# Kernel optimization log

Hardware: AMD Instinct MI355X
Metric: run time of the kernel (lower is better)

## Reference

```python
import jax, jax.numpy as jnp
import numpy as np

ENC_DIM = 512
QUERY_DIM = 1024
ATTN_DIM = 128
CONV_CH = 32
KERNEL = 31
B, T = 64, 2048


def setup_inputs() -> dict:
    key = jax.random.key(0)
    ks = jax.random.split(key, 9)
    s = 0.02
    encoder_outputs = jax.random.normal(ks[0], (B, T, ENC_DIM), dtype=jnp.float32)
    decoder_hidden = jax.random.normal(ks[1], (B, QUERY_DIM), dtype=jnp.float32)
    prev_attention = jax.random.uniform(ks[2], (B, T), dtype=jnp.float32)
    prev_attention = prev_attention / jnp.sum(prev_attention, axis=1, keepdims=True)
    Wq = jax.random.normal(ks[3], (QUERY_DIM, ATTN_DIM), dtype=jnp.float32) * s
    Wk = jax.random.normal(ks[4], (ENC_DIM, ATTN_DIM), dtype=jnp.float32) * s
    conv_w = jax.random.normal(ks[5], (CONV_CH, 1, KERNEL), dtype=jnp.float32) * s  # OIH
    conv_b = jax.random.normal(ks[6], (CONV_CH,), dtype=jnp.float32) * s
    Wloc = jax.random.normal(ks[7], (CONV_CH, ATTN_DIM), dtype=jnp.float32) * s
    v = jax.random.normal(ks[8], (ATTN_DIM,), dtype=jnp.float32) * s
    return {"encoder_outputs": encoder_outputs, "decoder_hidden": decoder_hidden,
            "prev_attention": prev_attention, "Wq": Wq, "Wk": Wk,
            "conv_w": conv_w, "conv_b": conv_b, "Wloc": Wloc, "v": v}


def reference(encoder_outputs, decoder_hidden, prev_attention, Wq, Wk, conv_w, conv_b, Wloc, v):
    # query: [B, 1, A]
    query = (decoder_hidden @ Wq)[:, None, :]
    # keys: [B, T, A]
    keys = jnp.einsum('bte,ea->bta', encoder_outputs, Wk)
    # location conv: prev_attention [B, T] -> [B, 1, T] -> [B, C, T], SAME padding
    pad = (KERNEL - 1) // 2
    loc = jax.lax.conv_general_dilated(
        prev_attention[:, None, :], conv_w,
        window_strides=(1,), padding=[(pad, pad)],
        dimension_numbers=('NCH', 'OIH', 'NCH'))
    loc = loc + conv_b[None, :, None]
    # [B, T, C] -> [B, T, A]
    location_term = jnp.einsum('bct,ca->bta', loc, Wloc)
    energy = jnp.einsum('bta,a->bt', jnp.tanh(keys + query + location_term), v)
    return jax.nn.softmax(energy, axis=1)
```

## Files before the change

### kernel.cpp

```cpp
#include <hip/hip_runtime.h>
#include <hip/hip_bf16.h>

#define B_  64
#define T_  2048
#define E_  512
#define Q_  1024
#define A_  128
#define C_  32
#define KW_ 31

using bf16x8 = __attribute__((ext_vector_type(8))) short;
using f32x4  = __attribute__((ext_vector_type(4))) float;

__device__ __forceinline__ short f2bf(float f) {
  union { float f; unsigned u; } x; x.f = f;
  unsigned r = x.u + 0x7fffu + ((x.u >> 16) & 1u);
  return (short)(r >> 16);
}

__device__ __forceinline__ bf16x8 pack8(float4 a, float4 b) {
  union { bf16x8 v; __hip_bfloat162 h[4]; } u;
  u.h[0] = __float22bfloat162_rn(make_float2(a.x, a.y));
  u.h[1] = __float22bfloat162_rn(make_float2(a.z, a.w));
  u.h[2] = __float22bfloat162_rn(make_float2(b.x, b.y));
  u.h[3] = __float22bfloat162_rn(make_float2(b.z, b.w));
  return u.v;
}

__device__ __forceinline__ float fast_tanh(float x) {
  float e2 = __expf(2.f * x);
  return 1.f - 2.f * __builtin_amdgcn_rcpf(e2 + 1.f);
}

__device__ __forceinline__ void gload16(const void* g, void* l) {
  __builtin_amdgcn_global_load_lds(
      (const __attribute__((address_space(1))) unsigned int*)g,
      (__attribute__((address_space(3))) unsigned int*)l, 16, 0, 0);
}

__global__ __launch_bounds__(256) void prep_kernel(
    const float* __restrict__ dh, const float* __restrict__ Wq,
    const float* __restrict__ conv_b, const float* __restrict__ Wloc,
    const float* __restrict__ Wk,
    unsigned short* __restrict__ wkf, unsigned short* __restrict__ wlocf,
    float* __restrict__ q2p)
{
  int blk = blockIdx.x;
  int tid = threadIdx.x;
  if (blk < 512) {
    __shared__ float part[128];
    int b = blk >> 3, kq = blk & 7;
    int a = tid & 127, kh = tid >> 7;
    const float* dhr = dh + b * Q_ + kq * 128 + kh * 64;
    const float* wq  = Wq + (size_t)(kq * 128 + kh * 64) * A_ + a;
    float s = 0.f;
    #pragma unroll 8
    for (int k = 0; k < 64; ++k) s += dhr[k] * wq[(size_t)k * A_];
    if (kh) part[a] = s;
    __syncthreads();
    if (!kh) {
      s += part[a];
      if (kq == 0) {
        float t = 0.f;
        #pragma unroll 8
        for (int c = 0; c < C_; ++c) t += conv_b[c] * Wloc[c * A_ + a];
        s += t;
      }
      q2p[(kq * B_ + b) * A_ + a] = s;
    }
  } else if (blk < 544) {
    int wave = tid >> 6, lane = tid & 63;
    int g = (blk - 512) * 4 + wave;
    int ks = g >> 3, nt = g & 7;
    int lg = lane >> 4, lr = lane & 15;
    bf16x8 o;
    #pragma unroll
    for (int j = 0; j < 8; ++j)
      o[j] = f2bf(Wk[(ks * 32 + lg * 8 + j) * A_ + nt * 16 + lr]);
    *(bf16x8*)(wkf + ((size_t)g * 64 + lane) * 8) = o;
  } else {
    int wave = tid >> 6, lane = tid & 63;
    int g = (blk - 544) * 4 + wave;
    int lg = lane >> 4, lr = lane & 15;
    bf16x8 o;
    #pragma unroll
    for (int j = 0; j < 8; ++j)
      o[j] = f2bf(Wloc[(lg * 8 + j) * A_ + g * 16 + lr]);
    *(bf16x8*)(wlocf + ((size_t)g * 64 + lane) * 8) = o;
  }
}

__global__ __launch_bounds__(256, 4) void energy_kernel(
    const float* __restrict__ enc, const float* __restrict__ prev,
    const float* __restrict__ conv_w,
    const unsigned short* __restrict__ wkfall,
    const float* __restrict__ q2p, const float* __restrict__ vvec,
    float* __restrict__ outexp, float* __restrict__ psum)
{
  __shared__ unsigned short sB0[4096];
  __shared__ unsigned short sB1[4096];
  __shared__ float sprev[160];
  __shared__ float scw[KW_][C_];
  __shared__ unsigned short slocb[128][C_];
  __shared__ float swsum[4];

  int tid = threadIdx.x;
  int m0 = blockIdx.x * 128;
  int b  = m0 >> 11, t0 = m0 & (T_ - 1);

  for (int i = tid; i < 158; i += 256) {
    int t = t0 - 15 + i;
    sprev[i] = (t >= 0 && t < T_) ? prev[b * T_ + t] : 0.f;
  }
  for (int i = tid; i < KW_ * C_; i += 256) {
    int j = i >> 5, c = i & 31;
    scw[j][c] = conv_w[c * KW_ + j];
  }
  __syncthreads();
  {
    int tl = tid >> 1, ch0 = (tid & 1) * 16;
    float acc[16];
    #pragma unroll
    for (int c = 0; c < 16; ++c) acc[c] = 0.f;
    for (int j = 0; j < KW_; ++j) {
      float p = sprev[tl + j];
      #pragma unroll
      for (int c = 0; c < 16; ++c) acc[c] += p * scw[j][ch0 + c];
    }
    unsigned int* dstp = (unsigned int*)&slocb[tl][ch0];
    #pragma unroll
    for (int c = 0; c < 16; c += 2)
      dstp[c >> 1] = ((unsigned int)(unsigned short)f2bf(acc[c + 1]) << 16)
                   | (unsigned short)f2bf(acc[c]);
  }
  __syncthreads();

  int wave = tid >> 6, lane = tid & 63;
  int lg = lane >> 4, lr = lane & 15;
  int wm = m0 + wave * 32;

  const float* encRow0 = enc + (size_t)(wm + lr) * E_ + lg * 8;
  const float* encRow1 = encRow0 + 16 * E_;

  #define STAGE(slice, buf) do {                                              \
    const unsigned short* s_ = wkfall + (size_t)(slice) * 4096 + wave * 512 + lane * 8; \
    gload16(s_,        &buf[wave * 512]);                                     \
    gload16(s_ + 2048, &buf[(4 + wave) * 512]);                               \
  } while (0)

  f32x4 acc0[8], acc1[8];
  #pragma unroll
  for (int i = 0; i < 8; ++i) { acc0[i] = (f32x4){0,0,0,0}; acc1[i] = (f32x4){0,0,0,0}; }

  float4 aA0, aA1, aA2, aA3, aB0, aB1, aB2, aB3;

  STAGE(0, sB0);
  __builtin_amdgcn_sched_barrier(0);
  aA0 = *(const float4*)(encRow0);     aA1 = *(const float4*)(encRow0 + 4);
  aA2 = *(const float4*)(encRow1);     aA3 = *(const float4*)(encRow1 + 4);
  asm volatile("s_waitcnt vmcnt(4)" ::: "memory");
  __builtin_amdgcn_sched_barrier(0);
  __builtin_amdgcn_s_barrier();

  #pragma unroll 1
  for (int i = 0; i < 8; ++i) {
    STAGE(2 * i + 1, sB1);
    __builtin_amdgcn_sched_barrier(0);
    {
      const float* r0 = encRow0 + (2 * i + 1) * 32;
      const float* r1 = encRow1 + (2 * i + 1) * 32;
      aB0 = *(const float4*)(r0); aB1 = *(const float4*)(r0 + 4);
      aB2 = *(const float4*)(r1); aB3 = *(const float4*)(r1 + 4);
    }
    {
      bf16x8 af0 = pack8(aA0, aA1), af1 = pack8(aA2, aA3);
      #pragma unroll
      for (int nt = 0; nt < 8; ++nt) {
        bf16x8 bfr = *(const bf16x8*)&sB0[nt * 512 + lane * 8];
        acc0[nt] = __builtin_amdgcn_mfma_f32_16x16x32_bf16(af0, bfr, acc0[nt], 0, 0, 0);
        acc1[nt] = __builtin_amdgcn_mfma_f32_16x16x32_bf16(af1, bfr, acc1[nt], 0, 0, 0);
      }
    }
    asm volatile("s_waitcnt vmcnt(4) lgkmcnt(0)" ::: "memory");
    __builtin_amdgcn_sched_barrier(0);
    __builtin_amdgcn_s_barrier();

    STAGE(2 * i + 2, sB0);
    __builtin_amdgcn_sched_barrier(0);
    if (i < 7) {
      const float* r0 = encRow0 + (2 * i + 2) * 32;
      const float* r1 = encRow1 + (2 * i + 2) * 32;
      aA0 = *(const float4*)(r0); aA1 = *(const float4*)(r0 + 4);
      aA2 = *(const float4*)(r1); aA3 = *(const float4*)(r1 + 4);
    }
    {
      bf16x8 af0 = pack8(aB0, aB1), af1 = pack8(aB2, aB3);
      #pragma unroll
      for (int nt = 0; nt < 8; ++nt) {
        bf16x8 bfr = *(const bf16x8*)&sB1[nt * 512 + lane * 8];
        acc0[nt] = __builtin_amdgcn_mfma_f32_16x16x32_bf16(af0, bfr, acc0[nt], 0, 0, 0);
        acc1[nt] = __builtin_amdgcn_mfma_f32_16x16x32_bf16(af1, bfr, acc1[nt], 0, 0, 0);
      }
    }
    if (i < 7) { asm volatile("s_waitcnt vmcnt(4) lgkmcnt(0)" ::: "memory"); }
    else       { asm volatile("s_waitcnt vmcnt(0) lgkmcnt(0)" ::: "memory"); }
    __builtin_amdgcn_sched_barrier(0);
    __builtin_amdgcn_s_barrier();
  }

  {
    int lrow = wave * 32 + lr;
    bf16x8 af0 = *(const bf16x8*)&slocb[lrow][lg * 8];
    bf16x8 af1 = *(const bf16x8*)&slocb[lrow + 16][lg * 8];
    #pragma unroll
    for (int nt = 0; nt < 8; ++nt) {
      bf16x8 bfr = *(const bf16x8*)&sB0[nt * 512 + lane * 8];
      acc0[nt] = __builtin_amdgcn_mfma_f32_16x16x32_bf16(af0, bfr, acc0[nt], 0, 0, 0);
      acc1[nt] = __builtin_amdgcn_mfma_f32_16x16x32_bf16(af1, bfr, acc1[nt], 0, 0, 0);
    }
  }

  float qv[8], vv[8];
  #pragma unroll
  for (int nt = 0; nt < 8; ++nt) {
    int n = nt * 16 + lr;
    float s = 0.f;
    #pragma unroll
    for (int p = 0; p < 8; ++p) s += q2p[(p * B_ + b) * A_ + n];
    qv[nt] = s;
    vv[nt] = vvec[n];
  }
  float ssum = 0.f;
  #pragma unroll
  for (int f = 0; f < 2; ++f) {
    f32x4* acc = f ? acc1 : acc0;
    float p0 = 0, p1 = 0, p2 = 0, p3 = 0;
    #pragma unroll
    for (int nt = 0; nt < 8; ++nt) {
      p0 += fast_tanh(acc[nt][0] + qv[nt]) * vv[nt];
      p1 += fast_tanh(acc[nt][1] + qv[nt]) * vv[nt];
      p2 += fast_tanh(acc[nt][2] + qv[nt]) * vv[nt];
      p3 += fast_tanh(acc[nt][3] + qv[nt]) * vv[nt];
    }
    #pragma unroll
    for (int off = 1; off < 16; off <<= 1) {
      p0 += __shfl_xor(p0, off, 64);
      p1 += __shfl_xor(p1, off, 64);
      p2 += __shfl_xor(p2, off, 64);
      p3 += __shfl_xor(p3, off, 64);
    }
    float e0 = __expf(p0), e1 = __expf(p1), e2 = __expf(p2), e3 = __expf(p3);
    ssum += (e0 + e1) + (e2 + e3);
    if (lr == 0)
      *(float4*)(outexp + wm + f * 16 + lg * 4) = make_float4(e0, e1, e2, e3);
  }
  ssum += __shfl_xor(ssum, 16, 64);
  ssum += __shfl_xor(ssum, 32, 64);
  if (lane == 0) swsum[wave] = ssum;
  __syncthreads();
  if (tid == 0)
    psum[b * 16 + (blockIdx.x & 15)] = (swsum[0] + swsum[1]) + (swsum[2] + swsum[3]);
}

__global__ __launch_bounds__(256) void norm_kernel(float* __restrict__ out,
                                                   const float* __restrict__ psum)
{
  int b = blockIdx.x, tid = threadIdx.x;
  float s = 0.f;
  #pragma unroll
  for (int p = 0; p < 16; ++p) s += psum[b * 16 + p];
  float inv = 1.f / s;
  float4* row = (float4*)(out + (size_t)b * T_);
  #pragma unroll
  for (int j = 0; j < 2; ++j) {
    float4 x = row[tid + j * 256];
    x.x *= inv; x.y *= inv; x.z *= inv; x.w *= inv;
    row[tid + j * 256] = x;
  }
}

extern "C" void kernel_launch(void* const* d_in, const int* in_sizes, int n_in,
                              void* d_out, int out_size, void* d_ws, size_t ws_size,
                              hipStream_t stream)
{
  const float* enc   = (const float*)d_in[0];
  const float* dh    = (const float*)d_in[1];
  const float* prev  = (const float*)d_in[2];
  const float* Wq    = (const float*)d_in[3];
  const float* Wk    = (const float*)d_in[4];
  const float* convw = (const float*)d_in[5];
  const float* convb = (const float*)d_in[6];
  const float* Wloc  = (const float*)d_in[7];
  const float* v     = (const float*)d_in[8];
  float* out = (float*)d_out;

  char* w = (char*)d_ws;
  unsigned short* wkf   = (unsigned short*)w;
  unsigned short* wlocf = (unsigned short*)(w + 131072);
  float*          q2p   = (float*)(w + 139264);
  float*          psum  = (float*)(w + 401408);

  hipLaunchKernelGGL(prep_kernel, dim3(546), dim3(256), 0, stream,
                     dh, Wq, convb, Wloc, Wk, wkf, wlocf, q2p);
  hipLaunchKernelGGL(energy_kernel, dim3(1024), dim3(256), 0, stream,
                     enc, prev, convw, wkf, q2p, v, out, psum);
  hipLaunchKernelGGL(norm_kernel, dim3(64), dim3(256), 0, stream, out, psum);
}
```

Measured before the change: 72.73 us.

## Prefetch two K-slices of encoder rows per load and overlap with conv prologue

Hoists the first weight-slice stage and encoder-row loads ahead of the location-conv prologue so global latency overlaps the conv compute. Encoder A-fragments are now loaded two K-slices (64 floats) at a time, giving deeper prefetch per iteration, and launch bounds drop to 3 blocks per CU to allow the extra registers. The waitcnt pattern changes to vmcnt(8), with a full vmcnt(0) drain after the second half. That drain may serialize loads, and lower occupancy may reduce latency hiding.

```diff
diff --git a/kernel.cpp b/kernel.cpp
--- a/kernel.cpp
+++ b/kernel.cpp
@@ -90,7 +90,7 @@
   }
 }
 
-__global__ __launch_bounds__(256, 4) void energy_kernel(
+__global__ __launch_bounds__(256, 3) void energy_kernel(
     const float* __restrict__ enc, const float* __restrict__ prev,
     const float* __restrict__ conv_w,
     const unsigned short* __restrict__ wkfall,
@@ -108,6 +108,28 @@
   int m0 = blockIdx.x * 128;
   int b  = m0 >> 11, t0 = m0 & (T_ - 1);
 
+  int wave = tid >> 6, lane = tid & 63;
+  int lg = lane >> 4, lr = lane & 15;
+  int wm = m0 + wave * 32;
+
+  const float* encRow0 = enc + (size_t)(wm + lr) * E_ + lg * 8;
+  const float* encRow1 = encRow0 + 16 * E_;
+
+  #define STAGE(slice, buf) do {                                              \
+    const unsigned short* s_ = wkfall + (size_t)(slice) * 4096 + wave * 512 + lane * 8; \
+    gload16(s_,        &buf[wave * 512]);                                     \
+    gload16(s_ + 2048, &buf[(4 + wave) * 512]);                               \
+  } while (0)
+
+  float4 fl0, fl1, fl2, fl3, fl4, fl5, fl6, fl7;
+  STAGE(0, sB0);
+  __builtin_amdgcn_sched_barrier(0);
+  fl0 = *(const float4*)(encRow0);      fl1 = *(const float4*)(encRow0 + 4);
+  fl4 = *(const float4*)(encRow0 + 32); fl5 = *(const float4*)(encRow0 + 36);
+  fl2 = *(const float4*)(encRow1);      fl3 = *(const float4*)(encRow1 + 4);
+  fl6 = *(const float4*)(encRow1 + 32); fl7 = *(const float4*)(encRow1 + 36);
+  __builtin_amdgcn_sched_barrier(0);
+
   for (int i = tid; i < 158; i += 256) {
     int t = t0 - 15 + i;
     sprev[i] = (t >= 0 && t < T_) ? prev[b * T_ + t] : 0.f;
@@ -135,75 +157,46 @@
   }
   __syncthreads();
 
-  int wave = tid >> 6, lane = tid & 63;
-  int lg = lane >> 4, lr = lane & 15;
-  int wm = m0 + wave * 32;
-
-  const float* encRow0 = enc + (size_t)(wm + lr) * E_ + lg * 8;
-  const float* encRow1 = encRow0 + 16 * E_;
-
-  #define STAGE(slice, buf) do {                                              \
-    const unsigned short* s_ = wkfall + (size_t)(slice) * 4096 + wave * 512 + lane * 8; \
-    gload16(s_,        &buf[wave * 512]);                                     \
-    gload16(s_ + 2048, &buf[(4 + wave) * 512]);                               \
-  } while (0)
-
   f32x4 acc0[8], acc1[8];
   #pragma unroll
   for (int i = 0; i < 8; ++i) { acc0[i] = (f32x4){0,0,0,0}; acc1[i] = (f32x4){0,0,0,0}; }
-
-  float4 aA0, aA1, aA2, aA3, aB0, aB1, aB2, aB3;
-
-  STAGE(0, sB0);
-  __builtin_amdgcn_sched_barrier(0);
-  aA0 = *(const float4*)(encRow0);     aA1 = *(const float4*)(encRow0 + 4);
-  aA2 = *(const float4*)(encRow1);     aA3 = *(const float4*)(encRow1 + 4);
-  asm volatile("s_waitcnt vmcnt(4)" ::: "memory");
-  __builtin_amdgcn_sched_barrier(0);
-  __builtin_amdgcn_s_barrier();
 
   #pragma unroll 1
   for (int i = 0; i < 8; ++i) {
+    bf16x8 af00 = pack8(fl0, fl1), af01 = pack8(fl2, fl3);
+    bf16x8 af10 = pack8(fl4, fl5), af11 = pack8(fl6, fl7);
+
     STAGE(2 * i + 1, sB1);
-    __builtin_amdgcn_sched_barrier(0);
-    {
-      const float* r0 = encRow0 + (2 * i + 1) * 32;
-      const float* r1 = encRow1 + (2 * i + 1) * 32;
-      aB0 = *(const float4*)(r0); aB1 = *(const float4*)(r0 + 4);
-      aB2 = *(const float4*)(r1); aB3 = *(const float4*)(r1 + 4);
-    }
-    {
-      bf16x8 af0 = pack8(aA0, aA1), af1 = pack8(aA2, aA3);
-      #pragma unroll
-      for (int nt = 0; nt < 8; ++nt) {
-        bf16x8 bfr = *(const bf16x8*)&sB0[nt * 512 + lane * 8];
-        acc0[nt] = __builtin_amdgcn_mfma_f32_16x16x32_bf16(af0, bfr, acc0[nt], 0, 0, 0);
-        acc1[nt] = __builtin_amdgcn_mfma_f32_16x16x32_bf16(af1, bfr, acc1[nt], 0, 0, 0);
-      }
-    }
-    asm volatile("s_waitcnt vmcnt(4) lgkmcnt(0)" ::: "memory");
-    __builtin_amdgcn_sched_barrier(0);
-    __builtin_amdgcn_s_barrier();
-
-    STAGE(2 * i + 2, sB0);
     __builtin_amdgcn_sched_barrier(0);
     if (i < 7) {
       const float* r0 = encRow0 + (2 * i + 2) * 32;
       const float* r1 = encRow1 + (2 * i + 2) * 32;
-      aA0 = *(const float4*)(r0); aA1 = *(const float4*)(r0 + 4);
-      aA2 = *(const float4*)(r1); aA3 = *(const float4*)(r1 + 4);
-    }
-    {
-      bf16x8 af0 = pack8(aB0, aB1), af1 = pack8(aB2, aB3);
-      #pragma unroll
-      for (int nt = 0; nt < 8; ++nt) {
-        bf16x8 bfr = *(const bf16x8*)&sB1[nt * 512 + lane * 8];
-        acc0[nt] = __builtin_amdgcn_mfma_f32_16x16x32_bf16(af0, bfr, acc0[nt], 0, 0, 0);
-        acc1[nt] = __builtin_amdgcn_mfma_f32_16x16x32_bf16(af1, bfr, acc1[nt], 0, 0, 0);
-      }
-    }
-    if (i < 7) { asm volatile("s_waitcnt vmcnt(4) lgkmcnt(0)" ::: "memory"); }
+      fl0 = *(const float4*)(r0);      fl1 = *(const float4*)(r0 + 4);
+      fl4 = *(const float4*)(r0 + 32); fl5 = *(const float4*)(r0 + 36);
+      fl2 = *(const float4*)(r1);      fl3 = *(const float4*)(r1 + 4);
+      fl6 = *(const float4*)(r1 + 32); fl7 = *(const float4*)(r1 + 36);
+    }
+    __builtin_amdgcn_sched_barrier(0);
+    #pragma unroll
+    for (int nt = 0; nt < 8; ++nt) {
+      bf16x8 bfr = *(const bf16x8*)&sB0[nt * 512 + lane * 8];
+      acc0[nt] = __builtin_amdgcn_mfma_f32_16x16x32_bf16(af00, bfr, acc0[nt], 0, 0, 0);
+      acc1[nt] = __builtin_amdgcn_mfma_f32_16x16x32_bf16(af01, bfr, acc1[nt], 0, 0, 0);
+    }
+    if (i < 7) { asm volatile("s_waitcnt vmcnt(8) lgkmcnt(0)" ::: "memory"); }
     else       { asm volatile("s_waitcnt vmcnt(0) lgkmcnt(0)" ::: "memory"); }
+    __builtin_amdgcn_sched_barrier(0);
+    __builtin_amdgcn_s_barrier();
+
+    STAGE(2 * i + 2, sB0);
+    __builtin_amdgcn_sched_barrier(0);
+    #pragma unroll
+    for (int nt = 0; nt < 8; ++nt) {
+      bf16x8 bfr = *(const bf16x8*)&sB1[nt * 512 + lane * 8];
+      acc0[nt] = __builtin_amdgcn_mfma_f32_16x16x32_bf16(af10, bfr, acc0[nt], 0, 0, 0);
+      acc1[nt] = __builtin_amdgcn_mfma_f32_16x16x32_bf16(af11, bfr, acc1[nt], 0, 0, 0);
+    }
+    asm volatile("s_waitcnt vmcnt(0) lgkmcnt(0)" ::: "memory");
     __builtin_amdgcn_sched_barrier(0);
     __builtin_amdgcn_s_barrier();
   }
```

New measurement: 91.77 us. 1.26x slower.
